# Optimization experiments

Measured on AMD Instinct MI355X. Metric: run time of the kernel, lower is better.

Reference implementation:

```python
import jax, jax.numpy as jnp
import numpy as np

B, L, D, H = 2, 2048, 1024, 16
HD = D // H  # head_dim = 64


def setup_inputs() -> dict:
    key = jax.random.key(0)
    k1, k2, k3 = jax.random.split(key, 3)
    x = jax.random.normal(k1, (B, L, D), dtype=jnp.float32)
    # nn.Linear(d_model, 3*d_model): weight [3D, D], bias [3D]
    lim = 1.0 / np.sqrt(D)
    W_qkv = jax.random.uniform(k2, (3 * D, D), dtype=jnp.float32, minval=-lim, maxval=lim)
    b_qkv = jax.random.uniform(k3, (3 * D,), dtype=jnp.float32, minval=-lim, maxval=lim)
    return {"x": x, "W_qkv": W_qkv, "b_qkv": b_qkv}


def reference(x, W_qkv, b_qkv):
    b, l, d = x.shape
    qkv = x @ W_qkv.T + b_qkv                      # [b, l, 3d]
    q, k, v = jnp.split(qkv, 3, axis=-1)           # each [b, l, d]
    # split heads: [b, l, h, hd]
    q = q.reshape(b, l, H, HD)
    k = k.reshape(b, l, H, HD)
    v = v.reshape(b, l, H, HD)
    scale = 1.0 / np.sqrt(HD).astype(np.float32)
    # scores [b, h, l, l]
    scores = jnp.einsum('bqhd,bkhd->bhqk', q, k) * scale
    attn = jax.nn.softmax(scores, axis=-1)
    out = jnp.einsum('bhqk,bkhd->bqhd', attn, v)   # [b, l, h, hd]
    return out.reshape(b, l, d)
```

## Files before the change

### kernel.cpp

```cpp
#include <hip/hip_runtime.h>

#define BATCH 2
#define SEQ 2048
#define DMODEL 1024
#define NH 16
#define HD 64
#define M_TOT (BATCH*SEQ)
#define N_TOT (3*DMODEL)
#define K_TOT (DMODEL)
#define NQK   (2*DMODEL)
#define QSCALE 0.18033688011112042f

typedef __attribute__((ext_vector_type(8)))  _Float16 f16x8;
typedef __attribute__((ext_vector_type(4)))  float    f32x4;
typedef __attribute__((ext_vector_type(16))) float    f32x16;

static __device__ __forceinline__ unsigned short f2h(float f) {
  _Float16 h = (_Float16)f;
  return __builtin_bit_cast(unsigned short, h);
}

static __device__ __forceinline__ f32x16 zero16() {
  f32x16 z;
  #pragma unroll
  for (int i = 0; i < 16; ++i) z[i] = 0.f;
  return z;
}

static __device__ __forceinline__ void async16(const unsigned short* g, unsigned short* l) {
  __builtin_amdgcn_global_load_lds(
      (const __attribute__((address_space(1))) unsigned*)g,
      (__attribute__((address_space(3))) unsigned*)l, 16, 0, 0);
}

static __device__ __forceinline__ void barrier_f() {
  asm volatile("" ::: "memory");
  __builtin_amdgcn_s_barrier();
  asm volatile("" ::: "memory");
}

__global__ __launch_bounds__(256) void cast_f16_2(
    const float* __restrict__ xsrc, const float* __restrict__ wsrc,
    unsigned short* __restrict__ xdst, unsigned short* __restrict__ wdst,
    int n8x, int n8tot)
{
  int i = blockIdx.x * 256 + threadIdx.x;
  if (i >= n8tot) return;
  const float* src;
  unsigned short* dst;
  int idx;
  if (i < n8x) { src = xsrc; dst = xdst; idx = i; }
  else         { src = wsrc; dst = wdst; idx = i - n8x; }
  float4 v0 = ((const float4*)src)[2*idx];
  float4 v1 = ((const float4*)src)[2*idx + 1];
  uint4 pk;
  pk.x = (unsigned)f2h(v0.x) | ((unsigned)f2h(v0.y) << 16);
  pk.y = (unsigned)f2h(v0.z) | ((unsigned)f2h(v0.w) << 16);
  pk.z = (unsigned)f2h(v1.x) | ((unsigned)f2h(v1.y) << 16);
  pk.w = (unsigned)f2h(v1.z) | ((unsigned)f2h(v1.w) << 16);
  ((uint4*)dst)[idx] = pk;
}

__global__ __launch_bounds__(256) void qkv_gemm_mfma(
    const unsigned short* __restrict__ Xh,
    const unsigned short* __restrict__ Wh,
    const float* __restrict__ bias,
    unsigned short* __restrict__ QK,
    unsigned short* __restrict__ VT)
{
  __shared__ unsigned short As[3][128][32];
  __shared__ unsigned short Bs[3][128][32];

  const int tid  = threadIdx.x;
  const int wave = tid >> 6;
  const int lane = tid & 63;
  const int l15  = lane & 15;
  const int quad = lane >> 4;

  const int lin = blockIdx.x + blockIdx.y * 24;
  const int c   = lin & 7;
  const int w   = lin >> 3;
  const int bxl = (c & 1) * 12 + (w % 12);
  const int byl = (c >> 1) * 8 + (w / 12);

  const bool isV = (bxl >= (NQK/128));
  const int n0 = (isV ? (bxl - NQK/128) : bxl) * 128;
  const int m0 = byl * 128;

  const unsigned short* Arows = isV ? (Wh + (size_t)(NQK + n0) * K_TOT)
                                    : (Xh + (size_t)m0 * K_TOT);
  const unsigned short* Brows = isV ? (Xh + (size_t)m0 * K_TOT)
                                    : (Wh + (size_t)n0 * K_TOT);

  const int srow = tid >> 2;
  const int skc  = (tid & 3) * 8;
  const unsigned short* Ag0 = Arows + (size_t)srow * K_TOT + skc;
  const unsigned short* Ag1 = Arows + (size_t)(64 + srow) * K_TOT + skc;
  const unsigned short* Bg0 = Brows + (size_t)srow * K_TOT + skc;
  const unsigned short* Bg1 = Brows + (size_t)(64 + srow) * K_TOT + skc;
  unsigned short* Al = &As[0][0][0] + tid * 8;
  unsigned short* Bl = &Bs[0][0][0] + tid * 8;

  const int wm = (wave & 1) * 64;
  const int wn = (wave >> 1) * 64;

  f32x4 acc[4][4];
  #pragma unroll
  for (int i = 0; i < 4; ++i)
    #pragma unroll
    for (int j = 0; j < 4; ++j) acc[i][j] = (f32x4){0.f,0.f,0.f,0.f};

  auto STAGE = [&](int k0, int bb) {
    async16(Ag0 + k0, Al + bb*4096);
    async16(Ag1 + k0, Al + bb*4096 + 2048);
    async16(Bg0 + k0, Bl + bb*4096);
    async16(Bg1 + k0, Bl + bb*4096 + 2048);
  };

  auto COMPUTE = [&](int bb) {
    f16x8 af[4], bf[4];
    #pragma unroll
    for (int i = 0; i < 4; ++i)
      af[i] = *(const f16x8*)&As[bb][wm + i*16 + l15][quad*8];
    #pragma unroll
    for (int j = 0; j < 4; ++j)
      bf[j] = *(const f16x8*)&Bs[bb][wn + j*16 + l15][quad*8];
    #pragma unroll
    for (int i = 0; i < 4; ++i)
      #pragma unroll
      for (int j = 0; j < 4; ++j)
        acc[i][j] = __builtin_amdgcn_mfma_f32_16x16x32_f16(af[i], bf[j], acc[i][j], 0, 0, 0);
  };

  #define G_KSTEP(t, sb, cb) \
    asm volatile("s_waitcnt vmcnt(4)" ::: "memory"); \
    barrier_f(); \
    STAGE(((t)+2)*32, (sb)); \
    COMPUTE((cb));

  STAGE(0, 0);
  STAGE(32, 1);
  for (int t = 0; t < 30; t += 3) {
    G_KSTEP(t,   2, 0)
    G_KSTEP(t+1, 0, 1)
    G_KSTEP(t+2, 1, 2)
  }
  asm volatile("s_waitcnt vmcnt(4)" ::: "memory");
  barrier_f();
  COMPUTE(0);
  asm volatile("s_waitcnt vmcnt(0)" ::: "memory");
  barrier_f();
  COMPUTE(1);
  #undef G_KSTEP

  if (!isV) {
    const float sc = (n0 < DMODEL) ? QSCALE : 1.0f;
    float bv[4];
    #pragma unroll
    for (int j = 0; j < 4; ++j) bv[j] = bias[n0 + wn + j*16 + l15];
    #pragma unroll
    for (int i = 0; i < 4; ++i)
      #pragma unroll
      for (int j = 0; j < 4; ++j)
        #pragma unroll
        for (int r = 0; r < 4; ++r) {
          const size_t row = (size_t)(m0 + wm + i*16 + quad*4 + r);
          QK[row * NQK + n0 + wn + j*16 + l15] = f2h((acc[i][j][r] + bv[j]) * sc);
        }
  } else {
    const int bidx  = m0 >> 11;
    const int sbase = (m0 & 2047) + wn;
    #pragma unroll
    for (int i = 0; i < 4; ++i)
      #pragma unroll
      for (int r = 0; r < 4; ++r) {
        const int nn = n0 + wm + i*16 + quad*4 + r;
        const float bb = bias[NQK + nn];
        unsigned short* drow =
            VT + ((size_t)(bidx*NH + (nn >> 6)) * HD + (nn & 63)) * SEQ + sbase;
        #pragma unroll
        for (int j = 0; j < 4; ++j)
          drow[j*16 + l15] = f2h(acc[i][j][r] + bb);
      }
  }
}

__global__ __launch_bounds__(256) void attn_mfma3(
    const unsigned short* __restrict__ QK,
    const unsigned short* __restrict__ VT,
    float* __restrict__ out)
{
  __shared__ unsigned short Ks[2][64][64];
  __shared__ unsigned short Vs[2][64][64];
  __shared__ unsigned short Ps[4][32][72];
  __shared__ float Dn[4][32];

  const int tid  = threadIdx.x;
  const int wv   = tid >> 6;
  const int lane = tid & 63;
  const int l31  = lane & 31;
  const int h32  = lane >> 5;
  const int qsw  = l31 >> 3;

  const int lin = blockIdx.x + ((blockIdx.y + (blockIdx.z << 4)) << 4);
  const int logical = ((lin & 7) << 6) + (lin >> 3);
  const int qt   = logical & 15;
  const int head = logical >> 4;
  const int hh   = head & 15;
  const int b    = head >> 4;
  const int q0 = qt*128 + wv*32;

  f16x8 qf[4];
  {
    const unsigned short* qrow = QK + (size_t)(b*SEQ + q0 + l31) * NQK + hh*HD;
    #pragma unroll
    for (int f = 0; f < 4; ++f)
      qf[f] = *(const f16x8*)(qrow + f*16 + h32*8);
  }

  const unsigned short* Kg = QK + (size_t)b*SEQ*NQK + DMODEL + hh*HD;
  const unsigned short* Vg = VT + (size_t)(b*NH + hh) * HD * SEQ;

  const int sr = tid >> 3;
  const int sp = tid & 7;
  const int sg = ((sp - sr) & 7) * 8;

  const unsigned short* kg0 = Kg + (size_t)sr      * NQK + sg;
  const unsigned short* kg1 = Kg + (size_t)(sr+32) * NQK + sg;
  const unsigned short* vg0 = Vg + (size_t)sr      * SEQ + sg;
  const unsigned short* vg1 = Vg + (size_t)(sr+32) * SEQ + sg;
  unsigned short* kl = &Ks[0][0][0] + tid*8;
  unsigned short* vl = &Vs[0][0][0] + tid*8;

  f32x16 oacc[2];
  oacc[0] = zero16();
  oacc[1] = zero16();
  float dsv[4] = {0.f, 0.f, 0.f, 0.f};

  auto STAGE = [&](int kt, int bb) {
    const size_t krow = (size_t)kt * 64 * NQK;
    const int    kcol = kt * 64;
    async16(kg0 + krow, kl + bb*4096);
    async16(kg1 + krow, kl + bb*4096 + 2048);
    async16(vg0 + kcol, vl + bb*4096);
    async16(vg1 + kcol, vl + bb*4096 + 2048);
  };

  auto COMPUTE = [&](int bb) {
    const unsigned short* ks = &Ks[bb][0][0];
    const unsigned short* vs = &Vs[bb][0][0];

    f32x16 sa[2];
    sa[0] = zero16();
    sa[1] = zero16();
    __builtin_amdgcn_s_setprio(1);
    #pragma unroll
    for (int f = 0; f < 4; ++f) {
      const int g = f*2 + h32;
      #pragma unroll
      for (int kb = 0; kb < 2; ++kb) {
        const int row = kb*32 + l31;
        f16x8 kf = *(const f16x8*)(ks + row*64 + ((g + row) & 7) * 8);
        sa[kb] = __builtin_amdgcn_mfma_f32_32x32x16_f16(kf, qf[f], sa[kb], 0, 0, 0);
      }
    }
    __builtin_amdgcn_s_setprio(0);

    #pragma unroll
    for (int kb = 0; kb < 2; ++kb) {
      #pragma unroll
      for (int g4 = 0; g4 < 4; ++g4) {
        unsigned short hsv[4];
        #pragma unroll
        for (int r = 0; r < 4; ++r) {
          float p = exp2f(sa[kb][g4*4 + r]);
          dsv[r] += p;
          hsv[r] = f2h(p);
        }
        unsigned short* dst =
            &Ps[wv][l31][(((kb*4 + g4) ^ qsw) & 7) * 8 + h32*4];
        uint2 pk;
        pk.x = (unsigned)hsv[0] | ((unsigned)hsv[1] << 16);
        pk.y = (unsigned)hsv[2] | ((unsigned)hsv[3] << 16);
        *(uint2*)dst = pk;
      }
    }

    __builtin_amdgcn_s_setprio(1);
    #pragma unroll
    for (int f = 0; f < 4; ++f) {
      const int g = f*2 + h32;
      f16x8 pf = *(const f16x8*)&Ps[wv][l31][((g ^ qsw) & 7) * 8];
      #pragma unroll
      for (int jd = 0; jd < 2; ++jd) {
        const int row = jd*32 + l31;
        f16x8 vf = *(const f16x8*)(vs + row*64 + ((g + row) & 7) * 8);
        oacc[jd] = __builtin_amdgcn_mfma_f32_32x32x16_f16(pf, vf, oacc[jd], 0, 0, 0);
      }
    }
    __builtin_amdgcn_s_setprio(0);
  };

  #define A_STEP(kt, sb, cb) \
    STAGE((kt)+1, (sb)); \
    asm volatile("s_waitcnt vmcnt(4)" ::: "memory"); \
    barrier_f(); \
    COMPUTE((cb)); \
    barrier_f();

  STAGE(0, 0);
  for (int kt = 0; kt < 30; kt += 2) {
    A_STEP(kt,   1, 0)
    A_STEP(kt+1, 0, 1)
  }
  A_STEP(30, 1, 0)
  asm volatile("s_waitcnt vmcnt(0)" ::: "memory");
  barrier_f();
  COMPUTE(1);
  #undef A_STEP

  float dsum = (dsv[0] + dsv[1]) + (dsv[2] + dsv[3]);
  dsum += __shfl_xor(dsum, 32, 64);
  Dn[wv][l31] = 1.f / dsum;

  #pragma unroll
  for (int jd = 0; jd < 2; ++jd) {
    #pragma unroll
    for (int g4 = 0; g4 < 4; ++g4) {
      #pragma unroll
      for (int r = 0; r < 4; ++r) {
        const int qrow = g4*8 + h32*4 + r;
        const float oval = oacc[jd][g4*4 + r] * Dn[wv][qrow];
        out[(size_t)(b*SEQ + q0 + qrow) * DMODEL + hh*HD + jd*32 + l31] = oval;
      }
    }
  }
}

extern "C" void kernel_launch(void* const* d_in, const int* in_sizes, int n_in,
                              void* d_out, int out_size, void* d_ws, size_t ws_size,
                              hipStream_t stream) {
  const float* x    = (const float*)d_in[0];
  const float* W    = (const float*)d_in[1];
  const float* bias = (const float*)d_in[2];
  float* out = (float*)d_out;

  unsigned short* qk = (unsigned short*)d_ws;
  unsigned short* vt = qk + (size_t)M_TOT * NQK;
  unsigned short* xh = vt + (size_t)BATCH * NH * HD * SEQ;
  unsigned short* wh = xh + (size_t)M_TOT * K_TOT;

  const int n8x = M_TOT*K_TOT/8;
  const int n8w = N_TOT*K_TOT/8;
  cast_f16_2<<<(n8x + n8w + 255)/256, 256, 0, stream>>>(x, W, xh, wh, n8x, n8x + n8w);

  dim3 g1(N_TOT/128, M_TOT/128);
  qkv_gemm_mfma<<<g1, 256, 0, stream>>>(xh, wh, bias, qk, vt);

  dim3 g2(SEQ/128, NH, BATCH);
  attn_mfma3<<<g2, 256, 0, stream>>>(qk, vt, out);
}
```

Measured before the change: 183.2 us.

## Software-pipeline attention loop: overlap next tile's QK^T with current softmax and PV

Restructures the flash-attention inner loop so the QK^T MFMAs for tile t+1 are issued before the exp/softmax and PV MFMAs of tile t. V fragments are loaded into registers alongside the scores, so each LDS buffer can be released earlier and the exp work can overlap with matrix ops. This adds register pressure from the double score and V fragment sets, which may hurt occupancy or cause spills. The prologue and epilogue are unrolled by hand to handle the 32 tiles.

```diff
diff --git a/kernel.cpp b/kernel.cpp
--- a/kernel.cpp
+++ b/kernel.cpp
@@ -232,10 +232,18 @@
   unsigned short* kl = &Ks[0][0][0] + tid*8;
   unsigned short* vl = &Vs[0][0][0] + tid*8;
 
+  const unsigned short* k0p = &Ks[0][0][0];
+  const unsigned short* k1p = &Ks[1][0][0];
+  const unsigned short* v0p = &Vs[0][0][0];
+  const unsigned short* v1p = &Vs[1][0][0];
+
   f32x16 oacc[2];
   oacc[0] = zero16();
   oacc[1] = zero16();
   float dsv[4] = {0.f, 0.f, 0.f, 0.f};
+
+  f32x16 saA[2], saB[2];
+  f16x8  vrA[4][2], vrB[4][2];
 
   auto STAGE = [&](int kt, int bb) {
     const size_t krow = (size_t)kt * 64 * NQK;
@@ -246,13 +254,9 @@
     async16(vg1 + kcol, vl + bb*4096 + 2048);
   };
 
-  auto COMPUTE = [&](int bb) {
-    const unsigned short* ks = &Ks[bb][0][0];
-    const unsigned short* vs = &Vs[bb][0][0];
-
-    f32x16 sa[2];
-    sa[0] = zero16();
-    sa[1] = zero16();
+  auto QKPH = [&](const unsigned short* ksp, f32x16 (&sc)[2]) {
+    sc[0] = zero16();
+    sc[1] = zero16();
     __builtin_amdgcn_s_setprio(1);
     #pragma unroll
     for (int f = 0; f < 4; ++f) {
@@ -260,12 +264,26 @@
       #pragma unroll
       for (int kb = 0; kb < 2; ++kb) {
         const int row = kb*32 + l31;
-        f16x8 kf = *(const f16x8*)(ks + row*64 + ((g + row) & 7) * 8);
-        sa[kb] = __builtin_amdgcn_mfma_f32_32x32x16_f16(kf, qf[f], sa[kb], 0, 0, 0);
+        f16x8 kf = *(const f16x8*)(ksp + row*64 + ((g + row) & 7) * 8);
+        sc[kb] = __builtin_amdgcn_mfma_f32_32x32x16_f16(kf, qf[f], sc[kb], 0, 0, 0);
       }
     }
     __builtin_amdgcn_s_setprio(0);
-
+  };
+
+  auto VLD = [&](const unsigned short* vsp, f16x8 (&vr)[4][2]) {
+    #pragma unroll
+    for (int f = 0; f < 4; ++f) {
+      const int g = f*2 + h32;
+      #pragma unroll
+      for (int jd = 0; jd < 2; ++jd) {
+        const int row = jd*32 + l31;
+        vr[f][jd] = *(const f16x8*)(vsp + row*64 + ((g + row) & 7) * 8);
+      }
+    }
+  };
+
+  auto SMPV = [&](f32x16 (&sa)[2], f16x8 (&vr)[4][2]) {
     #pragma unroll
     for (int kb = 0; kb < 2; ++kb) {
       #pragma unroll
@@ -285,39 +303,50 @@
         *(uint2*)dst = pk;
       }
     }
-
     __builtin_amdgcn_s_setprio(1);
     #pragma unroll
     for (int f = 0; f < 4; ++f) {
       const int g = f*2 + h32;
       f16x8 pf = *(const f16x8*)&Ps[wv][l31][((g ^ qsw) & 7) * 8];
       #pragma unroll
-      for (int jd = 0; jd < 2; ++jd) {
-        const int row = jd*32 + l31;
-        f16x8 vf = *(const f16x8*)(vs + row*64 + ((g + row) & 7) * 8);
-        oacc[jd] = __builtin_amdgcn_mfma_f32_32x32x16_f16(pf, vf, oacc[jd], 0, 0, 0);
-      }
+      for (int jd = 0; jd < 2; ++jd)
+        oacc[jd] = __builtin_amdgcn_mfma_f32_32x32x16_f16(pf, vr[f][jd], oacc[jd], 0, 0, 0);
     }
     __builtin_amdgcn_s_setprio(0);
   };
 
-  #define A_STEP(kt, sb, cb) \
-    STAGE((kt)+1, (sb)); \
-    asm volatile("s_waitcnt vmcnt(4)" ::: "memory"); \
-    barrier_f(); \
-    COMPUTE((cb)); \
+  STAGE(0, 0);
+  STAGE(1, 1);
+  asm volatile("s_waitcnt vmcnt(4)" ::: "memory");
+  barrier_f();
+  QKPH(k0p, saA); VLD(v0p, vrA);
+  barrier_f();
+  for (int t = 1; t <= 27; t += 2) {
+    STAGE(t + 1, 0);
+    asm volatile("s_waitcnt vmcnt(4)" ::: "memory");
     barrier_f();
-
-  STAGE(0, 0);
-  for (int kt = 0; kt < 30; kt += 2) {
-    A_STEP(kt,   1, 0)
-    A_STEP(kt+1, 0, 1)
-  }
-  A_STEP(30, 1, 0)
+    QKPH(k1p, saB); VLD(v1p, vrB); SMPV(saA, vrA);
+    barrier_f();
+    STAGE(t + 2, 1);
+    asm volatile("s_waitcnt vmcnt(4)" ::: "memory");
+    barrier_f();
+    QKPH(k0p, saA); VLD(v0p, vrA); SMPV(saB, vrB);
+    barrier_f();
+  }
+  STAGE(30, 0);
+  asm volatile("s_waitcnt vmcnt(4)" ::: "memory");
+  barrier_f();
+  QKPH(k1p, saB); VLD(v1p, vrB); SMPV(saA, vrA);
+  barrier_f();
+  STAGE(31, 1);
+  asm volatile("s_waitcnt vmcnt(4)" ::: "memory");
+  barrier_f();
+  QKPH(k0p, saA); VLD(v0p, vrA); SMPV(saB, vrB);
+  barrier_f();
   asm volatile("s_waitcnt vmcnt(0)" ::: "memory");
   barrier_f();
-  COMPUTE(1);
-  #undef A_STEP
+  QKPH(k1p, saB); VLD(v1p, vrB); SMPV(saA, vrA);
+  SMPV(saB, vrB);
 
   float dsum = (dsv[0] + dsv[1]) + (dsv[2] + dsv[3]);
   dsum += __shfl_xor(dsum, 32, 64);
```

Result: slower. 210.0 us (+14.7%).
